# Kernel optimization log

Hardware: AMD Instinct MI355X
Metric: run time of the kernel (lower is better)

The kernel has to match this reference:

```python
import jax, jax.numpy as jnp
import numpy as np

N = 100000      # nodes
E = 1600000     # edges
G = 64          # graphs in batch
H = 128         # hidden (== num_features)
L = 4           # num_layers
C = 16          # num_classes
NCAND = 100000  # candidate edges
BN_EPS = 1e-5


def setup_inputs() -> dict:
    key = jax.random.key(0)
    ks = jax.random.split(key, 24)
    s = 0.05
    inp = {}
    inp["x"] = jax.random.normal(ks[0], (N, H), dtype=jnp.float32)
    inp["edge_index"] = jax.random.randint(ks[1], (2, E), 0, N)
    inp["batch"] = jnp.sort(jax.random.randint(ks[2], (N,), 0, G))
    inp["candidate_edges"] = jax.random.randint(ks[3], (2, NCAND), 0, N)
    # GIN conv params, stacked over L layers (all layers are H->H since num_features==hidden)
    inp["cW1"] = jax.random.normal(ks[4], (L, H, H), dtype=jnp.float32) * s
    inp["cb1"] = jnp.zeros((L, H), jnp.float32)
    inp["cW2"] = jax.random.normal(ks[5], (L, H, H), dtype=jnp.float32) * s
    inp["cb2"] = jnp.zeros((L, H), jnp.float32)
    inp["cgamma"] = jnp.ones((L, H), jnp.float32)
    inp["cbeta"] = jnp.zeros((L, H), jnp.float32)
    inp["ceps"] = jnp.zeros((L,), jnp.float32)  # train_eps=True, init 0
    # node classifier: L*H -> 2H -> H -> H -> C (dropout is identity in eval)
    inp["ncW1"] = jax.random.normal(ks[6], (L * H, 2 * H), dtype=jnp.float32) * s
    inp["ncb1"] = jnp.zeros((2 * H,), jnp.float32)
    inp["ncW2"] = jax.random.normal(ks[7], (2 * H, H), dtype=jnp.float32) * s
    inp["ncb2"] = jnp.zeros((H,), jnp.float32)
    inp["ncW3"] = jax.random.normal(ks[8], (H, H), dtype=jnp.float32) * s
    inp["ncb3"] = jnp.zeros((H,), jnp.float32)
    inp["ncW4"] = jax.random.normal(ks[9], (H, C), dtype=jnp.float32) * s
    inp["ncb4"] = jnp.zeros((C,), jnp.float32)
    # edge predictor: 2*L*H -> 2H -> H -> 1
    inp["epW1"] = jax.random.normal(ks[10], (2 * L * H, 2 * H), dtype=jnp.float32) * s
    inp["epb1"] = jnp.zeros((2 * H,), jnp.float32)
    inp["epW2"] = jax.random.normal(ks[11], (2 * H, H), dtype=jnp.float32) * s
    inp["epb2"] = jnp.zeros((H,), jnp.float32)
    inp["epW3"] = jax.random.normal(ks[12], (H, 1), dtype=jnp.float32) * s
    inp["epb3"] = jnp.zeros((1,), jnp.float32)
    return inp


def _forward(x, cW1, cb1, cW2, cb2, cgamma, cbeta, ceps,
             ncW1, ncb1, ncW2, ncb2, ncW3, ncb3, ncW4, ncb4,
             epW1, epb1, epW2, epb2, epW3, epb3,
             edge_index, batch, candidate_edges):
    src, dst = edge_index[0], edge_index[1]
    h = x
    xs = []
    for l in range(L):
        # GIN: (1+eps)*x_i + sum_{j->i} x_j  (scatter-add over destination nodes)
        agg = jax.ops.segment_sum(h[src], dst, num_segments=N)
        z = (1.0 + ceps[l]) * h + agg
        z = jax.nn.relu(z @ cW1[l] + cb1[l])
        z = jax.nn.relu(z @ cW2[l] + cb2[l])
        # BatchNorm1d (training-mode batch statistics, biased variance)
        mu = z.mean(axis=0)
        var = jnp.var(z, axis=0)
        h = (z - mu) * jax.lax.rsqrt(var + BN_EPS) * cgamma[l] + cbeta[l]
        xs.append(h)
    emb = jnp.concatenate(xs, axis=-1)  # [N, L*H]
    # global mean pool over graphs
    sums = jax.ops.segment_sum(emb, batch, num_segments=G)
    cnt = jax.ops.segment_sum(jnp.ones((N, 1), emb.dtype), batch, num_segments=G)
    gemb = sums / jnp.maximum(cnt, 1.0)  # [G, L*H]
    t = jax.nn.relu(gemb @ ncW1 + ncb1)
    t = jax.nn.relu(t @ ncW2 + ncb2)
    t = jax.nn.relu(t @ ncW3 + ncb3)
    class_output = jax.nn.log_softmax(t @ ncW4 + ncb4, axis=1)  # [G, C]
    # link prediction: gather node embeddings per candidate edge
    ef = jnp.concatenate([emb[candidate_edges[0]], emb[candidate_edges[1]]], axis=1)  # [NC, 2*L*H]
    u = jax.nn.relu(ef @ epW1 + epb1)
    u = jax.nn.relu(u @ epW2 + epb2)
    edge_scores = jax.nn.sigmoid((u @ epW3 + epb3).squeeze(-1))  # [NC]
    return class_output, edge_scores


def reference(x, cW1, cb1, cW2, cb2, cgamma, cbeta, ceps,
              ncW1, ncb1, ncW2, ncb2, ncW3, ncb3, ncW4, ncb4,
              epW1, epb1, epW2, epb2, epW3, epb3,
              edge_index, batch, candidate_edges):
    return _forward(x, cW1, cb1, cW2, cb2, cgamma, cbeta, ceps,
                    ncW1, ncb1, ncW2, ncb2, ncW3, ncb3, ncW4, ncb4,
                    epW1, epb1, epW2, epb2, epW3, epb3,
                    edge_index, batch, candidate_edges)
```

## Files before the change

### kernel.cpp

```cpp
#include <hip/hip_runtime.h>
#include <math.h>

#define NN 100000
#define EE 1600000
#define GG 64
#define HH 128
#define LL 4
#define CCLS 16
#define NC 100000
#define NB 49
#define LDK 40
#define LDA2 136
#define LDC 260

typedef __attribute__((ext_vector_type(8))) short bf16x8;
typedef __attribute__((ext_vector_type(4))) float f32x4;

__device__ __forceinline__ unsigned short f2bf(float x) {
  union { float f; unsigned int u; } v; v.f = x;
  unsigned int r = v.u + 0x7fffu + ((v.u >> 16) & 1u);
  return (unsigned short)(r >> 16);
}
__device__ __forceinline__ float bl(unsigned u) {
  union { unsigned u; float f; } v; v.u = u << 16; return v.f;
}
__device__ __forceinline__ float bh(unsigned u) {
  union { unsigned u; float f; } v; v.u = u & 0xffff0000u; return v.f;
}

__global__ void hist_kernel(const int* __restrict__ dst, int* __restrict__ cnt, int E) {
  int e = blockIdx.x * 256 + threadIdx.x;
  if (e < E) atomicAdd(&cnt[dst[e]], 1);
}

__global__ __launch_bounds__(256) void scan_p1(const int* __restrict__ cnt,
                                               int* __restrict__ bsum, int n) {
  __shared__ int red[256];
  int tid = threadIdx.x;
  int base = blockIdx.x * 1024 + tid * 4;
  int s = 0;
  if (base + 3 < n) {
    int4 v = *(const int4*)(cnt + base);
    s = v.x + v.y + v.z + v.w;
  } else {
    for (int i = 0; i < 4; ++i) if (base + i < n) s += cnt[base + i];
  }
  red[tid] = s;
  __syncthreads();
  for (int st = 128; st >= 1; st >>= 1) {
    if (tid < st) red[tid] += red[tid + st];
    __syncthreads();
  }
  if (tid == 0) bsum[blockIdx.x] = red[0];
}

__global__ void scan_p2(int* __restrict__ bsum, int* __restrict__ rowptr,
                        int* __restrict__ bcursor, int nb, int n) {
  __shared__ int buf[128];
  int tid = threadIdx.x;
  int v = (tid < nb) ? bsum[tid] : 0;
  buf[tid] = v;
  __syncthreads();
  for (int off = 1; off < 128; off <<= 1) {
    int t = (tid >= off) ? buf[tid - off] : 0;
    __syncthreads();
    buf[tid] += t;
    __syncthreads();
  }
  if (tid < nb) bsum[tid] = buf[tid] - v;
  if (tid == 127) rowptr[n] = buf[127];
  __syncthreads();
  if (tid < NB) bcursor[tid] = bsum[2 * tid];
}

__global__ __launch_bounds__(256) void scan_p3(const int* __restrict__ cnt,
                                               const int* __restrict__ bsum,
                                               int* __restrict__ rowptr,
                                               int* __restrict__ cursor, int n) {
  __shared__ int red[256];
  int tid = threadIdx.x;
  int base = blockIdx.x * 1024 + tid * 4;
  int v[4] = {0, 0, 0, 0};
  if (base + 3 < n) {
    int4 t = *(const int4*)(cnt + base);
    v[0] = t.x; v[1] = t.y; v[2] = t.z; v[3] = t.w;
  } else {
    for (int i = 0; i < 4; ++i) if (base + i < n) v[i] = cnt[base + i];
  }
  int s = v[0] + v[1] + v[2] + v[3];
  red[tid] = s;
  __syncthreads();
  for (int off = 1; off < 256; off <<= 1) {
    int t = (tid >= off) ? red[tid - off] : 0;
    __syncthreads();
    red[tid] += t;
    __syncthreads();
  }
  int run = bsum[blockIdx.x] + red[tid] - s;
  int4 o;
  o.x = run; o.y = run + v[0]; o.z = o.y + v[1]; o.w = o.z + v[2];
  if (base + 3 < n) {
    *(int4*)(rowptr + base) = o;
    *(int4*)(cursor + base) = o;
  } else {
    int oo[4] = {o.x, o.y, o.z, o.w};
    for (int i = 0; i < 4; ++i)
      if (base + i < n) { rowptr[base + i] = oo[i]; cursor[base + i] = oo[i]; }
  }
}

__global__ __launch_bounds__(256) void partition_kernel(const int* __restrict__ src,
                                                        const int* __restrict__ dst,
                                                        int* __restrict__ bcursor,
                                                        int2* __restrict__ pairs, int E) {
  __shared__ int sS[4096];
  __shared__ int sD[4096];
  __shared__ int hist[NB];
  __shared__ int base[NB];
  int tid = threadIdx.x;
  int base_e = blockIdx.x * 4096;
  int cnt = min(4096, E - base_e);
  if (tid < NB) hist[tid] = 0;
  for (int i = tid * 4; i < cnt; i += 1024) {
    if (i + 3 < cnt) {
      *(int4*)(sS + i) = *(const int4*)(src + base_e + i);
      *(int4*)(sD + i) = *(const int4*)(dst + base_e + i);
    } else {
      for (int k = i; k < cnt; ++k) { sS[k] = src[base_e + k]; sD[k] = dst[base_e + k]; }
    }
  }
  __syncthreads();
  for (int i = tid; i < cnt; i += 256) atomicAdd(&hist[sD[i] >> 11], 1);
  __syncthreads();
  if (tid < NB) {
    base[tid] = atomicAdd(&bcursor[tid], hist[tid]);
    hist[tid] = 0;
  }
  __syncthreads();
  for (int i = tid; i < cnt; i += 256) {
    int d = sD[i];
    int b = d >> 11;
    int off = atomicAdd(&hist[b], 1);
    pairs[base[b] + off] = make_int2(sS[i], d);
  }
}

__global__ __launch_bounds__(256) void scatter_csr(const int2* __restrict__ pairs,
                                                   const int* __restrict__ rowptr,
                                                   int* __restrict__ cursor,
                                                   int* __restrict__ csr_src) {
  int b = blockIdx.x % 56;
  int slice = blockIdx.x / 56;
  if (b >= NB) return;
  int start = rowptr[b * 2048];
  int endn = min((b + 1) * 2048, NN);
  int end = rowptr[endn];
  for (int i = start + slice * 256 + threadIdx.x; i < end; i += 8 * 256) {
    int2 p = pairs[i];
    int pos = atomicAdd(&cursor[p.y], 1);
    csr_src[pos] = p.x;
  }
}

__global__ void f2b4_kernel(const float* __restrict__ in, unsigned short* __restrict__ out, int n4) {
  int i = blockIdx.x * 256 + threadIdx.x;
  if (i >= n4) return;
  float4 v = ((const float4*)in)[i];
  unsigned short r[4] = {f2bf(v.x), f2bf(v.y), f2bf(v.z), f2bf(v.w)};
  *(uint2*)(out + (size_t)i * 4) = *(uint2*)r;
}

__global__ void conv_weights(const float* __restrict__ cW1, const float* __restrict__ cW2,
                             unsigned short* __restrict__ WT1, unsigned short* __restrict__ WT2,
                             const float* __restrict__ epW1, unsigned short* __restrict__ W1T,
                             const float* __restrict__ epW2, unsigned short* __restrict__ W2T) {
  int idx = blockIdx.x * 256 + threadIdx.x;
  if (idx < LL * 16384) {
    int l = idx >> 14, r = idx & 16383, k = r >> 7, n = r & 127;
    WT1[l * 16384 + n * 128 + k] = f2bf(cW1[idx]);
    WT2[l * 16384 + n * 128 + k] = f2bf(cW2[idx]);
  } else if (idx < LL * 16384 + 262144) {
    int j = idx - LL * 16384;
    int k = j >> 8, n = j & 255;
    W1T[(size_t)n * 1024 + k] = f2bf(epW1[j]);
  } else if (idx < LL * 16384 + 262144 + 32768) {
    int j = idx - LL * 16384 - 262144;
    int k = j >> 7, n = j & 127;
    W2T[(size_t)n * 256 + k] = f2bf(epW2[j]);
  }
}

__global__ void aggregate_bf16(const unsigned short* __restrict__ h16, int ld,
                               const int* __restrict__ rowptr,
                               const int* __restrict__ csr_src,
                               const float* __restrict__ ceps_l,
                               unsigned short* __restrict__ out, int n) {
  int wave = threadIdx.x >> 6;
  int lane = threadIdx.x & 63;
  int sub = lane >> 4;
  int li = lane & 15;
  int node = blockIdx.x * 16 + wave * 4 + sub;
  if (node >= n) return;
  int c8 = li * 8;
  float eps1 = 1.0f + *ceps_l;
  float acc[8] = {};
  int b = rowptr[node], e = rowptr[node + 1];
  int j = b;
  for (; j + 8 <= e; j += 8) {
    uint4 u[8];
#pragma unroll
    for (int t = 0; t < 8; ++t) {
      int s = csr_src[j + t];
      u[t] = *(const uint4*)(h16 + (size_t)s * ld + c8);
    }
#pragma unroll
    for (int t = 0; t < 8; ++t) {
      acc[0] += bl(u[t].x); acc[1] += bh(u[t].x);
      acc[2] += bl(u[t].y); acc[3] += bh(u[t].y);
      acc[4] += bl(u[t].z); acc[5] += bh(u[t].z);
      acc[6] += bl(u[t].w); acc[7] += bh(u[t].w);
    }
  }
  for (; j < e; ++j) {
    int s = csr_src[j];
    uint4 u = *(const uint4*)(h16 + (size_t)s * ld + c8);
    acc[0] += bl(u.x); acc[1] += bh(u.x);
    acc[2] += bl(u.y); acc[3] += bh(u.y);
    acc[4] += bl(u.z); acc[5] += bh(u.z);
    acc[6] += bl(u.w); acc[7] += bh(u.w);
  }
  uint4 hu = *(const uint4*)(h16 + (size_t)node * ld + c8);
  acc[0] = fmaf(eps1, bl(hu.x), acc[0]); acc[1] = fmaf(eps1, bh(hu.x), acc[1]);
  acc[2] = fmaf(eps1, bl(hu.y), acc[2]); acc[3] = fmaf(eps1, bh(hu.y), acc[3]);
  acc[4] = fmaf(eps1, bl(hu.z), acc[4]); acc[5] = fmaf(eps1, bh(hu.z), acc[5]);
  acc[6] = fmaf(eps1, bl(hu.w), acc[6]); acc[7] = fmaf(eps1, bh(hu.w), acc[7]);
  unsigned short o[8];
#pragma unroll
  for (int i = 0; i < 8; ++i) o[i] = f2bf(acc[i]);
  *(uint4*)(out + (size_t)node * 128 + c8) = *(uint4*)o;
}

__global__ __launch_bounds__(256) void trunk_fused(
    const unsigned short* __restrict__ A16,
    const unsigned short* __restrict__ W1T, const float* __restrict__ b1,
    const unsigned short* __restrict__ W2T, const float* __restrict__ b2,
    float* __restrict__ bnsum, float* __restrict__ bnsumsq,
    unsigned short* __restrict__ C16, int M) {
  __shared__ unsigned short As[128 * LDA2];
  __shared__ unsigned short Bs[128 * LDK];
  const int tid = threadIdx.x;
  const int bm = blockIdx.x * 128;
  const int lane = tid & 63;
  const int wave = tid >> 6;
  const int wr = (wave >> 1) << 6;
  const int wc = (wave & 1) << 6;
  const int ar = tid >> 1;
  const int ah = (tid & 1) << 4;
  int gra = bm + ar; if (gra >= M) gra = M - 1;
  const unsigned short* Arow = A16 + (size_t)gra * 128;
  const int mrow = lane & 15;
  const int kq = (lane >> 4) << 3;
  f32x4 acc[4][4] = {};

#pragma unroll
  for (int ks = 0; ks < 4; ++ks) {
    const int k0 = ks << 5;
    const uint4* s = (const uint4*)(Arow + k0 + ah);
    *(uint4*)(As + ar * LDA2 + k0 + ah) = s[0];
    *(uint4*)(As + ar * LDA2 + k0 + ah + 8) = s[1];
  }
  uint4 p0 = *(const uint4*)(W1T + (size_t)ar * 128 + ah);
  uint4 p1 = *(const uint4*)(W1T + (size_t)ar * 128 + ah + 8);
  for (int ks = 0; ks < 4; ++ks) {
    const int k0 = ks << 5;
    *(uint4*)(Bs + ar * LDK + ah) = p0;
    *(uint4*)(Bs + ar * LDK + ah + 8) = p1;
    __syncthreads();
    if (ks < 3) {
      p0 = *(const uint4*)(W1T + (size_t)ar * 128 + k0 + 32 + ah);
      p1 = *(const uint4*)(W1T + (size_t)ar * 128 + k0 + 32 + ah + 8);
    }
    bf16x8 af[4], bfv[4];
#pragma unroll
    for (int t = 0; t < 4; ++t)
      af[t] = *(const bf16x8*)(As + (wr + t * 16 + mrow) * LDA2 + k0 + kq);
#pragma unroll
    for (int t = 0; t < 4; ++t)
      bfv[t] = *(const bf16x8*)(Bs + (wc + t * 16 + mrow) * LDK + kq);
#pragma unroll
    for (int mt = 0; mt < 4; ++mt)
#pragma unroll
      for (int nt = 0; nt < 4; ++nt)
        acc[mt][nt] = __builtin_amdgcn_mfma_f32_16x16x32_bf16(af[mt], bfv[nt], acc[mt][nt], 0, 0, 0);
    __syncthreads();
  }
  const int crow = (lane >> 4) << 2;
  const int ccol = lane & 15;
#pragma unroll
  for (int nt = 0; nt < 4; ++nt) {
    int c = wc + nt * 16 + ccol;
    float bz = b1[c];
#pragma unroll
    for (int mt = 0; mt < 4; ++mt) {
      int rl = wr + mt * 16 + crow;
#pragma unroll
      for (int i = 0; i < 4; ++i)
        As[(rl + i) * LDA2 + c] = f2bf(fmaxf(acc[mt][nt][i] + bz, 0.f));
    }
  }
#pragma unroll
  for (int mt = 0; mt < 4; ++mt)
#pragma unroll
    for (int nt = 0; nt < 4; ++nt)
      acc[mt][nt] = (f32x4){0.f, 0.f, 0.f, 0.f};
  p0 = *(const uint4*)(W2T + (size_t)ar * 128 + ah);
  p1 = *(const uint4*)(W2T + (size_t)ar * 128 + ah + 8);
  __syncthreads();
  for (int ks = 0; ks < 4; ++ks) {
    const int k0 = ks << 5;
    *(uint4*)(Bs + ar * LDK + ah) = p0;
    *(uint4*)(Bs + ar * LDK + ah + 8) = p1;
    __syncthreads();
    if (ks < 3) {
      p0 = *(const uint4*)(W2T + (size_t)ar * 128 + k0 + 32 + ah);
      p1 = *(const uint4*)(W2T + (size_t)ar * 128 + k0 + 32 + ah + 8);
    }
    bf16x8 af[4], bfv[4];
#pragma unroll
    for (int t = 0; t < 4; ++t)
      af[t] = *(const bf16x8*)(As + (wr + t * 16 + mrow) * LDA2 + k0 + kq);
#pragma unroll
    for (int t = 0; t < 4; ++t)
      bfv[t] = *(const bf16x8*)(Bs + (wc + t * 16 + mrow) * LDK + kq);
#pragma unroll
    for (int mt = 0; mt < 4; ++mt)
#pragma unroll
      for (int nt = 0; nt < 4; ++nt)
        acc[mt][nt] = __builtin_amdgcn_mfma_f32_16x16x32_bf16(af[mt], bfv[nt], acc[mt][nt], 0, 0, 0);
    __syncthreads();
  }
#pragma unroll
  for (int nt = 0; nt < 4; ++nt) {
    int c = wc + nt * 16 + ccol;
    float bz = b2[c];
    float s = 0.f, q = 0.f;
#pragma unroll
    for (int mt = 0; mt < 4; ++mt) {
      int rbase = bm + wr + mt * 16 + crow;
#pragma unroll
      for (int i = 0; i < 4; ++i) {
        int r = rbase + i;
        if (r < M) {
          float v = fmaxf(acc[mt][nt][i] + bz, 0.f);
          C16[(size_t)r * 128 + c] = f2bf(v);
          s += v; q += v * v;
        }
      }
    }
    s += __shfl_xor(s, 16, 64);
    s += __shfl_xor(s, 32, 64);
    q += __shfl_xor(q, 16, 64);
    q += __shfl_xor(q, 32, 64);
    if (lane < 16) {
      atomicAdd(&bnsum[c], s);
      atomicAdd(&bnsumsq[c], q);
    }
  }
}

__global__ __launch_bounds__(512) void ep_fused(
    const unsigned short* __restrict__ emb16, const int* __restrict__ cand,
    const unsigned short* __restrict__ W1T ,
    const float* __restrict__ b1,
    const unsigned short* __restrict__ W2T ,
    const float* __restrict__ b2, const float* __restrict__ epW3,
    const float* __restrict__ epb3,
    float* __restrict__ out, int M) {
  __shared__ unsigned short smem[128 * LDC];
  __shared__ float sDot[128];
  const int AOFF = 0;
  const int BOFF = 2 * 128 * LDK;
  const int tid = threadIdx.x;
  const int bm = blockIdx.x * 128;
  const int lane = tid & 63;
  const int wave = tid >> 6;
  const int wr = (wave >> 2) << 6;
  const int wc = (wave & 3) << 6;
  f32x4 acc[4][4] = {};
  const int ar = tid >> 2;
  const int ah = (tid & 3) << 3;
  int gra = bm + ar; if (gra >= M) gra = M - 1;
  const int node0 = cand[gra];
  const int node1 = cand[NC + gra];
  const int br = tid >> 1;
  const int bh8 = (tid & 1) << 4;
  const unsigned short* Brow = W1T + (size_t)br * 1024 + bh8;
  const int mrow = lane & 15;
  const int kq = (lane >> 4) << 3;

  if (tid < 128) sDot[tid] = 0.f;
  {
    uint4 a = *(const uint4*)(emb16 + (size_t)node0 * 512 + ah);
    uint4 b0 = *(const uint4*)(Brow);
    uint4 b1v = *(const uint4*)(Brow + 8);
    *(uint4*)(smem + AOFF + ar * LDK + ah) = a;
    *(uint4*)(smem + BOFF + br * LDK + bh8) = b0;
    *(uint4*)(smem + BOFF + br * LDK + bh8 + 8) = b1v;
  }
  __syncthreads();
  for (int ks = 0; ks < 32; ++ks) {
    const int cur = ks & 1;
    unsigned short* Ac = smem + AOFF + cur * (128 * LDK);
    unsigned short* Bc = smem + BOFF + cur * (256 * LDK);
    unsigned short* An = smem + AOFF + (cur ^ 1) * (128 * LDK);
    unsigned short* Bn = smem + BOFF + (cur ^ 1) * (256 * LDK);
    uint4 a, b0, b1v;
    if (ks < 31) {
      const int k1 = (ks + 1) << 5;
      int node = (k1 < 512) ? node0 : node1;
      a = *(const uint4*)(emb16 + (size_t)node * 512 + (k1 & 511) + ah);
      b0 = *(const uint4*)(Brow + k1);
      b1v = *(const uint4*)(Brow + k1 + 8);
    }
    bf16x8 af[4], bfv[4];
#pragma unroll
    for (int t = 0; t < 4; ++t)
      af[t] = *(const bf16x8*)(Ac + (wr + t * 16 + mrow) * LDK + kq);
#pragma unroll
    for (int t = 0; t < 4; ++t)
      bfv[t] = *(const bf16x8*)(Bc + (wc + t * 16 + mrow) * LDK + kq);
#pragma unroll
    for (int mt = 0; mt < 4; ++mt)
#pragma unroll
      for (int nt = 0; nt < 4; ++nt)
        acc[mt][nt] = __builtin_amdgcn_mfma_f32_16x16x32_bf16(af[mt], bfv[nt], acc[mt][nt], 0, 0, 0);
    if (ks < 31) {
      *(uint4*)(An + ar * LDK + ah) = a;
      *(uint4*)(Bn + br * LDK + bh8) = b0;
      *(uint4*)(Bn + br * LDK + bh8 + 8) = b1v;
      __syncthreads();
    }
  }
  __syncthreads();
  const int crow = (lane >> 4) << 2;
  const int ccol = lane & 15;
#pragma unroll
  for (int nt = 0; nt < 4; ++nt) {
    int c = wc + nt * 16 + ccol;
    float bz = b1[c];
#pragma unroll
    for (int mt = 0; mt < 4; ++mt) {
      int rl = wr + mt * 16 + crow;
#pragma unroll
      for (int i = 0; i < 4; ++i)
        smem[(rl + i) * LDC + c] = f2bf(fmaxf(acc[mt][nt][i] + bz, 0.f));
    }
  }
  __syncthreads();
  const int wr2 = (wave >> 1) << 5;
  const int wc2 = (wave & 1) << 6;
  f32x4 acc2[2][4] = {};
  for (int ks = 0; ks < 8; ++ks) {
    const int k0 = ks << 5;
    bf16x8 af[2], bfv[4];
#pragma unroll
    for (int t = 0; t < 2; ++t)
      af[t] = *(const bf16x8*)(smem + (wr2 + t * 16 + mrow) * LDC + k0 + kq);
#pragma unroll
    for (int t = 0; t < 4; ++t)
      bfv[t] = *(const bf16x8*)(W2T + (size_t)(wc2 + t * 16 + mrow) * 256 + k0 + kq);
#pragma unroll
    for (int mt = 0; mt < 2; ++mt)
#pragma unroll
      for (int nt = 0; nt < 4; ++nt)
        acc2[mt][nt] = __builtin_amdgcn_mfma_f32_16x16x32_bf16(af[mt], bfv[nt], acc2[mt][nt], 0, 0, 0);
  }
  float w3v[4], bz2[4];
#pragma unroll
  for (int nt = 0; nt < 4; ++nt) {
    int c = wc2 + nt * 16 + ccol;
    w3v[nt] = epW3[c];
    bz2[nt] = b2[c];
  }
#pragma unroll
  for (int mt = 0; mt < 2; ++mt) {
#pragma unroll
    for (int i = 0; i < 4; ++i) {
      int rl = wr2 + mt * 16 + crow + i;
      float p = 0.f;
#pragma unroll
      for (int nt = 0; nt < 4; ++nt)
        p = fmaf(fmaxf(acc2[mt][nt][i] + bz2[nt], 0.f), w3v[nt], p);
      atomicAdd(&sDot[rl], p);
    }
  }
  __syncthreads();
  if (tid < 128) {
    int r = bm + tid;
    if (r < M) out[r] = 1.f / (1.f + expf(-(sDot[tid] + epb3[0])));
  }
}

__global__ void bn_apply_bf16(const unsigned short* __restrict__ z,
                              const float* __restrict__ sum, const float* __restrict__ sumsq,
                              const float* __restrict__ gamma, const float* __restrict__ beta,
                              unsigned short* __restrict__ out, int n) {
  int idx = blockIdx.x * 256 + threadIdx.x;
  if (idx >= n * 16) return;
  int r = idx >> 4, c8 = (idx & 15) << 3;
  uint4 v = *(const uint4*)(z + (size_t)r * 128 + c8);
  float f[8] = {bl(v.x), bh(v.x), bl(v.y), bh(v.y), bl(v.z), bh(v.z), bl(v.w), bh(v.w)};
  const float inv_n = 1.0f / (float)NN;
  unsigned short o[8];
#pragma unroll
  for (int j = 0; j < 8; ++j) {
    int c = c8 + j;
    float mu = sum[c] * inv_n;
    float var = sumsq[c] * inv_n - mu * mu;
    float sc = rsqrtf(var + 1e-5f) * gamma[c];
    o[j] = f2bf((f[j] - mu) * sc + beta[c]);
  }
  *(uint4*)(out + (size_t)r * 512 + c8) = *(uint4*)o;
}

__global__ void bounds_kernel(const int* __restrict__ batch, int* __restrict__ gstart, int n) {
  int g = threadIdx.x;
  if (g > GG) return;
  int lo = 0, hi = n;
  while (lo < hi) {
    int mid = (lo + hi) >> 1;
    if (batch[mid] < g) lo = mid + 1; else hi = mid;
  }
  gstart[g] = lo;
}

__global__ __launch_bounds__(256) void pool_bf16(const unsigned short* __restrict__ emb16,
                                                 const int* __restrict__ gstart,
                                                 float* __restrict__ gsum) {
  int g = blockIdx.x;
  int chunk = blockIdx.y;
  int c2 = threadIdx.x * 2;
  int s = gstart[g], e = gstart[g + 1];
  int len = e - s;
  int per = (len + 7) >> 3;
  int r0 = s + chunk * per;
  int r1 = min(r0 + per, e);
  float ax = 0.f, ay = 0.f;
  for (int r = r0; r < r1; ++r) {
    unsigned u = *(const unsigned*)(emb16 + (size_t)r * 512 + c2);
    ax += bl(u); ay += bh(u);
  }
  if (r1 > r0) {
    atomicAdd(&gsum[g * 512 + c2], ax);
    atomicAdd(&gsum[g * 512 + c2 + 1], ay);
  }
}

__global__ __launch_bounds__(256) void nc_fused(
    const float* __restrict__ gsum, const int* __restrict__ gstart,
    const float* __restrict__ W1, const float* __restrict__ b1,
    const float* __restrict__ W2, const float* __restrict__ b2,
    const float* __restrict__ W3, const float* __restrict__ b3,
    const float* __restrict__ W4, const float* __restrict__ b4,
    float* __restrict__ out) {
  __shared__ float row[512];
  __shared__ float t1[256];
  __shared__ float t2[128];
  __shared__ float t3s[128];
  __shared__ float lg[16];
  int g = blockIdx.x;
  int tid = threadIdx.x;
  float inv = 1.0f / fmaxf((float)(gstart[g + 1] - gstart[g]), 1.0f);
  row[tid] = gsum[g * 512 + tid] * inv;
  row[tid + 256] = gsum[g * 512 + tid + 256] * inv;
  __syncthreads();
  {
    float acc = b1[tid];
#pragma unroll 8
    for (int k = 0; k < 512; ++k) acc = fmaf(row[k], W1[k * 256 + tid], acc);
    t1[tid] = fmaxf(acc, 0.f);
  }
  __syncthreads();
  if (tid < 128) {
    float acc = b2[tid];
#pragma unroll 8
    for (int k = 0; k < 256; ++k) acc = fmaf(t1[k], W2[k * 128 + tid], acc);
    t2[tid] = fmaxf(acc, 0.f);
  }
  __syncthreads();
  if (tid < 128) {
    float acc = b3[tid];
#pragma unroll 8
    for (int k = 0; k < 128; ++k) acc = fmaf(t2[k], W3[k * 128 + tid], acc);
    t3s[tid] = fmaxf(acc, 0.f);
  }
  __syncthreads();
  if (tid < 16) {
    float acc = b4[tid];
#pragma unroll 8
    for (int k = 0; k < 128; ++k) acc = fmaf(t3s[k], W4[k * 16 + tid], acc);
    lg[tid] = acc;
  }
  __syncthreads();
  if (tid < 16) {
    float v = lg[tid];
    float m = v;
    for (int j = 0; j < 16; ++j) m = fmaxf(m, lg[j]);
    float s = 0.f;
    for (int j = 0; j < 16; ++j) s += expf(lg[j] - m);
    out[g * 16 + tid] = v - m - logf(s);
  }
}

extern "C" void kernel_launch(void* const* d_in, const int* in_sizes, int n_in,
                              void* d_out, int out_size, void* d_ws, size_t ws_size,
                              hipStream_t stream) {
  const float* x = (const float*)d_in[0];
  const int* edge_index = (const int*)d_in[1];
  const int* batch = (const int*)d_in[2];
  const int* cand = (const int*)d_in[3];
  const float* cW1 = (const float*)d_in[4];
  const float* cb1 = (const float*)d_in[5];
  const float* cW2 = (const float*)d_in[6];
  const float* cb2 = (const float*)d_in[7];
  const float* cgamma = (const float*)d_in[8];
  const float* cbeta = (const float*)d_in[9];
  const float* ceps = (const float*)d_in[10];
  const float* ncW1 = (const float*)d_in[11];
  const float* ncb1 = (const float*)d_in[12];
  const float* ncW2 = (const float*)d_in[13];
  const float* ncb2 = (const float*)d_in[14];
  const float* ncW3 = (const float*)d_in[15];
  const float* ncb3 = (const float*)d_in[16];
  const float* ncW4 = (const float*)d_in[17];
  const float* ncb4 = (const float*)d_in[18];
  const float* epW1 = (const float*)d_in[19];
  const float* epb1 = (const float*)d_in[20];
  const float* epW2 = (const float*)d_in[21];
  const float* epb2 = (const float*)d_in[22];
  const float* epW3 = (const float*)d_in[23];
  const float* epb3 = (const float*)d_in[24];

  char* ws = (char*)d_ws;
  size_t off = 0;
  auto alloc = [&](size_t bytes) -> void* {
    off = (off + 255) & ~(size_t)255;
    void* p = ws + off;
    off += bytes;
    return p;
  };
  size_t zz_bytes = (size_t)NN * 4 + 512 * 4 + 512 * 4 + (size_t)GG * 512 * 4;
  char* zz = (char*)alloc(zz_bytes);
  int* cnt = (int*)zz;
  float* bnsum = (float*)(zz + (size_t)NN * 4);
  float* bnsumsq = bnsum + 512;
  float* gsum = bnsumsq + 512;
  int* rowptr = (int*)alloc((size_t)(NN + 1) * 4);
  int* cursor = (int*)alloc((size_t)NN * 4);
  int* csr_src = (int*)alloc((size_t)EE * 4);
  int2* pairs = (int2*)alloc((size_t)EE * 8);
  int* bsum = (int*)alloc(128 * 4);
  int* bcursor = (int*)alloc(64 * 4);
  unsigned short* x16 = (unsigned short*)alloc((size_t)NN * 128 * 2);
  unsigned short* g16a = (unsigned short*)alloc((size_t)NN * 128 * 2);
  unsigned short* emb16 = (unsigned short*)alloc((size_t)NN * 512 * 2);
  unsigned short* WT1 = (unsigned short*)alloc((size_t)LL * 16384 * 2);
  unsigned short* WT2 = (unsigned short*)alloc((size_t)LL * 16384 * 2);
  unsigned short* W1T = (unsigned short*)alloc((size_t)1024 * 256 * 2);
  unsigned short* W2T = (unsigned short*)alloc((size_t)256 * 128 * 2);
  int* gstart = (int*)alloc(65 * 4);

  const int* esrc = edge_index;
  const int* edst = edge_index + EE;
  const int nblk = (NN + 1023) / 1024;
  const int nech = (EE + 4095) / 4096;

  hipMemsetAsync(zz, 0, zz_bytes, stream);
  hist_kernel<<<(EE + 255) / 256, 256, 0, stream>>>(edst, cnt, EE);
  scan_p1<<<nblk, 256, 0, stream>>>(cnt, bsum, NN);
  scan_p2<<<1, 128, 0, stream>>>(bsum, rowptr, bcursor, nblk, NN);
  scan_p3<<<nblk, 256, 0, stream>>>(cnt, bsum, rowptr, cursor, NN);
  partition_kernel<<<nech, 256, 0, stream>>>(esrc, edst, bcursor, pairs, EE);
  scatter_csr<<<56 * 8, 256, 0, stream>>>(pairs, rowptr, cursor, csr_src);
  f2b4_kernel<<<(NN * 128 / 4 + 255) / 256, 256, 0, stream>>>(x, x16, NN * 128 / 4);
  conv_weights<<<(LL * 16384 + 262144 + 32768 + 255) / 256, 256, 0, stream>>>(
      cW1, cW2, WT1, WT2, epW1, W1T, epW2, W2T);

  for (int l = 0; l < LL; ++l) {
    const unsigned short* h16 = (l == 0) ? x16 : (emb16 + (size_t)(l - 1) * 128);
    int ld = (l == 0) ? 128 : 512;
    aggregate_bf16<<<(NN + 15) / 16, 256, 0, stream>>>(h16, ld, rowptr, csr_src, ceps + l, g16a, NN);
    trunk_fused<<<(NN + 127) / 128, 256, 0, stream>>>(
        g16a, WT1 + (size_t)l * 16384, cb1 + l * 128,
        WT2 + (size_t)l * 16384, cb2 + l * 128,
        bnsum + l * 128, bnsumsq + l * 128, g16a, NN);
    bn_apply_bf16<<<(NN * 16 + 255) / 256, 256, 0, stream>>>(
        g16a, bnsum + l * 128, bnsumsq + l * 128, cgamma + l * 128, cbeta + l * 128,
        emb16 + (size_t)l * 128, NN);
  }

  bounds_kernel<<<1, 128, 0, stream>>>(batch, gstart, NN);
  pool_bf16<<<dim3(GG, 8), 256, 0, stream>>>(emb16, gstart, gsum);
  nc_fused<<<GG, 256, 0, stream>>>(gsum, gstart, ncW1, ncb1, ncW2, ncb2, ncW3, ncb3,
                                   ncW4, ncb4, (float*)d_out);

  ep_fused<<<(NC + 127) / 128, 512, 0, stream>>>(
      emb16, cand, W1T, epb1, W2T, epb2, epW3, epb3,
      (float*)d_out + GG * CCLS, NC);
}
```

Before: 1.106 ms.

## Load edge-predictor GEMM operands directly from global memory, bypassing LDS staging

The first edge-predictor GEMM no longer stages gathered node embeddings and W1T tiles through double-buffered shared memory with a barrier per k-step. Each wave now loads its MFMA fragments straight from global memory (and cache), removing the synchronisation and LDS traffic. Launch bounds are raised to request 4 blocks per CU. The cost is redundant global and L2 reads, since each A and B fragment is now fetched by several waves instead of being shared through LDS, plus higher register pressure.

```diff
diff --git a/kernel.cpp b/kernel.cpp
--- a/kernel.cpp
+++ b/kernel.cpp
@@ -368,7 +368,7 @@
   }
 }
 
-__global__ __launch_bounds__(512) void ep_fused(
+__global__ __launch_bounds__(512, 4) void ep_fused(
     const unsigned short* __restrict__ emb16, const int* __restrict__ cand,
     const unsigned short* __restrict__ W1T ,
     const float* __restrict__ b1,
@@ -378,70 +378,70 @@
     float* __restrict__ out, int M) {
   __shared__ unsigned short smem[128 * LDC];
   __shared__ float sDot[128];
-  const int AOFF = 0;
-  const int BOFF = 2 * 128 * LDK;
   const int tid = threadIdx.x;
   const int bm = blockIdx.x * 128;
   const int lane = tid & 63;
   const int wave = tid >> 6;
   const int wr = (wave >> 2) << 6;
   const int wc = (wave & 3) << 6;
-  f32x4 acc[4][4] = {};
-  const int ar = tid >> 2;
-  const int ah = (tid & 3) << 3;
-  int gra = bm + ar; if (gra >= M) gra = M - 1;
-  const int node0 = cand[gra];
-  const int node1 = cand[NC + gra];
-  const int br = tid >> 1;
-  const int bh8 = (tid & 1) << 4;
-  const unsigned short* Brow = W1T + (size_t)br * 1024 + bh8;
   const int mrow = lane & 15;
   const int kq = (lane >> 4) << 3;
+  f32x4 acc[4][4] = {};
 
   if (tid < 128) sDot[tid] = 0.f;
+
+  int n0[4], n1[4];
+#pragma unroll
+  for (int t = 0; t < 4; ++t) {
+    int rr = bm + wr + t * 16 + mrow;
+    if (rr >= M) rr = M - 1;
+    n0[t] = cand[rr];
+    n1[t] = cand[NC + rr];
+  }
+  const unsigned short* pB[4];
+#pragma unroll
+  for (int t = 0; t < 4; ++t)
+    pB[t] = W1T + (size_t)(wc + t * 16 + mrow) * 1024 + kq;
+
   {
-    uint4 a = *(const uint4*)(emb16 + (size_t)node0 * 512 + ah);
-    uint4 b0 = *(const uint4*)(Brow);
-    uint4 b1v = *(const uint4*)(Brow + 8);
-    *(uint4*)(smem + AOFF + ar * LDK + ah) = a;
-    *(uint4*)(smem + BOFF + br * LDK + bh8) = b0;
-    *(uint4*)(smem + BOFF + br * LDK + bh8 + 8) = b1v;
-  }
-  __syncthreads();
-  for (int ks = 0; ks < 32; ++ks) {
-    const int cur = ks & 1;
-    unsigned short* Ac = smem + AOFF + cur * (128 * LDK);
-    unsigned short* Bc = smem + BOFF + cur * (256 * LDK);
-    unsigned short* An = smem + AOFF + (cur ^ 1) * (128 * LDK);
-    unsigned short* Bn = smem + BOFF + (cur ^ 1) * (256 * LDK);
-    uint4 a, b0, b1v;
-    if (ks < 31) {
-      const int k1 = (ks + 1) << 5;
-      int node = (k1 < 512) ? node0 : node1;
-      a = *(const uint4*)(emb16 + (size_t)node * 512 + (k1 & 511) + ah);
-      b0 = *(const uint4*)(Brow + k1);
-      b1v = *(const uint4*)(Brow + k1 + 8);
-    }
-    bf16x8 af[4], bfv[4];
-#pragma unroll
-    for (int t = 0; t < 4; ++t)
-      af[t] = *(const bf16x8*)(Ac + (wr + t * 16 + mrow) * LDK + kq);
-#pragma unroll
-    for (int t = 0; t < 4; ++t)
-      bfv[t] = *(const bf16x8*)(Bc + (wc + t * 16 + mrow) * LDK + kq);
-#pragma unroll
-    for (int mt = 0; mt < 4; ++mt)
-#pragma unroll
-      for (int nt = 0; nt < 4; ++nt)
-        acc[mt][nt] = __builtin_amdgcn_mfma_f32_16x16x32_bf16(af[mt], bfv[nt], acc[mt][nt], 0, 0, 0);
-    if (ks < 31) {
-      *(uint4*)(An + ar * LDK + ah) = a;
-      *(uint4*)(Bn + br * LDK + bh8) = b0;
-      *(uint4*)(Bn + br * LDK + bh8 + 8) = b1v;
-      __syncthreads();
-    }
-  }
-  __syncthreads();
+    const unsigned short* pA[4];
+#pragma unroll
+    for (int t = 0; t < 4; ++t) pA[t] = emb16 + (size_t)n0[t] * 512 + kq;
+#pragma unroll 4
+    for (int ks = 0; ks < 16; ++ks) {
+      const int k0 = ks << 5;
+      bf16x8 af[4], bfv[4];
+#pragma unroll
+      for (int t = 0; t < 4; ++t) af[t] = *(const bf16x8*)(pA[t] + k0);
+#pragma unroll
+      for (int t = 0; t < 4; ++t) bfv[t] = *(const bf16x8*)(pB[t] + k0);
+#pragma unroll
+      for (int mt = 0; mt < 4; ++mt)
+#pragma unroll
+        for (int nt = 0; nt < 4; ++nt)
+          acc[mt][nt] = __builtin_amdgcn_mfma_f32_16x16x32_bf16(af[mt], bfv[nt], acc[mt][nt], 0, 0, 0);
+    }
+  }
+  {
+    const unsigned short* pA[4];
+#pragma unroll
+    for (int t = 0; t < 4; ++t) pA[t] = emb16 + (size_t)n1[t] * 512 + kq;
+#pragma unroll 4
+    for (int ks = 0; ks < 16; ++ks) {
+      const int k0 = ks << 5;
+      bf16x8 af[4], bfv[4];
+#pragma unroll
+      for (int t = 0; t < 4; ++t) af[t] = *(const bf16x8*)(pA[t] + k0);
+#pragma unroll
+      for (int t = 0; t < 4; ++t) bfv[t] = *(const bf16x8*)(pB[t] + 512 + k0);
+#pragma unroll
+      for (int mt = 0; mt < 4; ++mt)
+#pragma unroll
+        for (int nt = 0; nt < 4; ++nt)
+          acc[mt][nt] = __builtin_amdgcn_mfma_f32_16x16x32_bf16(af[mt], bfv[nt], acc[mt][nt], 0, 0, 0);
+    }
+  }
+
   const int crow = (lane >> 4) << 2;
   const int ccol = lane & 15;
 #pragma unroll
```

Result: slower. 1.238 ms (+12.0%).
